# Kernel tuning notes

Hardware: AMD Instinct MI355X
Metric: run time of the kernel (lower is better)

## Reference

```python
import jax, jax.numpy as jnp
import numpy as np

EPS_BN = 1e-5
EPS_W = 1e-8


def setup_inputs() -> dict:
    key = jax.random.key(0)
    ks = jax.random.split(key, 6)
    B, N, S, D1, D2 = 8, 8192, 2048, 128, 256
    Cin = D1 + D2  # 384
    return {
        "points_position": jax.random.normal(ks[0], (B, 3, N), jnp.float32),
        "sampled_points_position": jax.random.normal(ks[1], (B, 3, S), jnp.float32),
        "skip_points_feature": jax.random.normal(ks[2], (B, D1, N), jnp.float32),
        "sampled_points_feature": jax.random.normal(ks[3], (B, D2, S), jnp.float32),
        "W1": jax.random.normal(ks[4], (256, Cin), jnp.float32) * 0.05,
        "b1": jnp.zeros((256,), jnp.float32),
        "g1": jnp.ones((256,), jnp.float32),
        "beta1": jnp.zeros((256,), jnp.float32),
        "W2": jax.random.normal(ks[5], (128, 256), jnp.float32) * 0.05,
        "b2": jnp.zeros((128,), jnp.float32),
        "g2": jnp.ones((128,), jnp.float32),
        "beta2": jnp.zeros((128,), jnp.float32),
    }


def _bn_relu(x, g, b):
    # train-mode BatchNorm1d over (batch, points) per channel, x: [B,N,C]
    mean = jnp.mean(x, axis=(0, 1), keepdims=True)
    var = jnp.mean(jnp.square(x - mean), axis=(0, 1), keepdims=True)  # biased var
    return jax.nn.relu((x - mean) * jax.lax.rsqrt(var + EPS_BN) * g + b)


def reference(points_position, sampled_points_position, skip_points_feature,
              sampled_points_feature, W1, b1, g1, beta1, W2, b2, g2, beta2):
    pos = points_position.transpose(0, 2, 1)            # [B,N,3]
    spos = sampled_points_position.transpose(0, 2, 1)   # [B,S,3]
    sfeat = sampled_points_feature.transpose(0, 2, 1)   # [B,S,D2]

    # squared pairwise distance [B,N,S]
    d = (jnp.sum(pos * pos, axis=-1, keepdims=True)
         - 2.0 * jnp.einsum("bnc,bsc->bns", pos, spos)
         + jnp.sum(spos * spos, axis=-1)[:, None, :])

    # 3 nearest neighbors (smallest distances)
    neg_d3, idx = jax.lax.top_k(-d, 3)                  # [B,N,3]
    d3 = -neg_d3
    w = 1.0 / (d3 + EPS_W)
    w = w / jnp.sum(w, axis=-1, keepdims=True)          # [B,N,3]

    gathered = jax.vmap(lambda f, i: f[i])(sfeat, idx)  # [B,N,3,D2]
    interp = jnp.einsum("bnk,bnkd->bnd", w, gathered)   # [B,N,D2]

    feat = jnp.concatenate([skip_points_feature.transpose(0, 2, 1), interp], axis=-1)  # [B,N,D1+D2]

    h = _bn_relu(jnp.einsum("bnc,oc->bno", feat, W1) + b1, g1, beta1)  # [B,N,256]
    h = _bn_relu(jnp.einsum("bnc,oc->bno", h, W2) + b2, g2, beta2)     # [B,N,128]
    return h.transpose(0, 2, 1)                          # [B,128,N]
```

## Files before the change

### kernel.cpp

```cpp
#include <hip/hip_runtime.h>

constexpr int BATCH = 8;
constexpr int NPT   = 8192;
constexpr int NSMP  = 2048;
constexpr int D1C   = 128;
constexpr int D2C   = 256;
constexpr int CIN   = 384;
constexpr int C1    = 256;
constexpr int C2    = 128;
constexpr int BN_TOTAL = BATCH * NPT;

constexpr int BM = 128, BK = 32;
constexpr int NRB = BN_TOTAL / BM;
constexpr int NRW = NRB * 2;

typedef __bf16 bf16x8 __attribute__((ext_vector_type(8)));
typedef short  s16x8  __attribute__((ext_vector_type(8)));
typedef float  f32x4  __attribute__((ext_vector_type(4)));

__device__ __forceinline__ unsigned short f2bf(float x) {
  unsigned u = __builtin_bit_cast(unsigned, x);
  u += 0x7fffu + ((u >> 16) & 1u);
  return (unsigned short)(u >> 16);
}
__device__ __forceinline__ float bf2f(unsigned short h) {
  return __builtin_bit_cast(float, (unsigned)h << 16);
}

__device__ __forceinline__ void gld_lds16(const void* g, void* l) {
  __builtin_amdgcn_global_load_lds(
      (const __attribute__((address_space(1))) void*)g,
      (__attribute__((address_space(3))) void*)l, 16, 0, 0);
}

__global__ void transpose_k(const float* __restrict__ in, float* __restrict__ out,
                            int rows, int cols, long inBatch, long outBatch) {
  __shared__ float tile[32][33];
  const float* inb = in + (size_t)blockIdx.z * inBatch;
  float* outb = out + (size_t)blockIdx.z * outBatch;
  int c0 = blockIdx.x * 32;
  int r0 = blockIdx.y * 32;
  int tx = threadIdx.x, ty = threadIdx.y;
#pragma unroll
  for (int i = 0; i < 32; i += 8) {
    int r = r0 + ty + i;
    tile[ty + i][tx] = inb[(size_t)r * cols + c0 + tx];
  }
  __syncthreads();
#pragma unroll
  for (int i = 0; i < 32; i += 8) {
    int c = c0 + ty + i;
    outb[(size_t)c * rows + r0 + tx] = tile[tx][ty + i];
  }
}

__global__ void skip_to_featB(const float* __restrict__ skip,
                              unsigned short* __restrict__ featB) {
  __shared__ float tile[32][33];
  int b = blockIdx.z;
  int n0 = blockIdx.x * 32;
  int d0 = blockIdx.y * 32;
  int tx = threadIdx.x, ty = threadIdx.y;
#pragma unroll
  for (int i = 0; i < 32; i += 8) {
    tile[ty + i][tx] = skip[((size_t)b * D1C + d0 + ty + i) * NPT + n0 + tx];
  }
  __syncthreads();
#pragma unroll
  for (int i = 0; i < 32; i += 8) {
    int n = n0 + ty + i;
    featB[((size_t)b * NPT + n) * CIN + d0 + tx] = f2bf(tile[tx][ty + i]);
  }
}

__global__ __launch_bounds__(256) void prep_misc(
    const float* __restrict__ spos, float* __restrict__ sposI, float4* __restrict__ qs4,
    const float* __restrict__ W1, unsigned short* __restrict__ W1h,
    const float* __restrict__ W2, unsigned short* __restrict__ W2h,
    int* __restrict__ flag_count) {
  int g = blockIdx.x * 256 + threadIdx.x;
  if (g == 0) *flag_count = 0;
  if (g < C1 * CIN) W1h[g] = f2bf(W1[g]);
  if (g < C2 * C1)  W2h[g] = f2bf(W2[g]);
  if (g < BATCH * NSMP) {
    int b = g >> 11, s = g & (NSMP - 1);
    const float* sp = spos + (size_t)b * 3 * NSMP;
    float x = sp[s], y = sp[NSMP + s], z = sp[2 * NSMP + s];
    sposI[(size_t)g * 3 + 0] = x;
    sposI[(size_t)g * 3 + 1] = y;
    sposI[(size_t)g * 3 + 2] = z;
    qs4[g] = make_float4(-2.f * x, -2.f * y, -2.f * z,
                         fmaf(x, x, fmaf(y, y, z * z)));
  }
}

constexpr int KWAVES = 8;
constexpr int SEGK = NSMP / KWAVES;

__device__ __forceinline__ void ins_med3(float kf, float& k0, float& k1,
                                         float& k2, float& k3) {
  float o0 = k0, o1 = k1, o2 = k2;
  k0 = fminf(kf, o0);
  k1 = __builtin_amdgcn_fmed3f(kf, o0, o1);
  k2 = __builtin_amdgcn_fmed3f(kf, o1, o2);
  k3 = __builtin_amdgcn_fmed3f(kf, o2, k3);
}

__global__ __launch_bounds__(512, 4) void knn_kernel(
    const float* __restrict__ pos,
    const float4* __restrict__ qs4g,
    const float* __restrict__ sposI,
    int* __restrict__ idx_out,
    float* __restrict__ wgt_out,
    int* __restrict__ flag_list,
    int* __restrict__ flag_count) {
  __shared__ float mk[KWAVES][4][64];

  int tid = threadIdx.x;
  int wave = tid >> 6, lane = tid & 63;
  int blk = blockIdx.x;
  int b = blk >> 7;
  int n = ((blk & 127) << 6) + lane;

  const float* pb = pos + (size_t)b * 3 * NPT;
  float px = pb[n], py = pb[NPT + n], pz = pb[2 * NPT + n];
  float pp = fmaf(px, px, fmaf(py, py, pz * pz));

  const float INF = __builtin_inff();
  float k0 = INF, k1 = INF, k2 = INF, k3 = INF;

  int s0 = wave * SEGK;
  int tv = 0;
  asm volatile("" : "+v"(tv));
  const float4* qseg = qs4g + (size_t)b * NSMP + s0 + tv;

#define KSTEP(Q, SS)                                                        \
  {                                                                         \
    float tt = (Q).w + pp;      \
    float d_ = fmaf(px, (Q).x, fmaf(py, (Q).y, fmaf(pz, (Q).z, tt)));       \
    unsigned ki_ = (__builtin_bit_cast(unsigned, d_) & 0xFFFFF800u) |       \
                   (unsigned)(SS);                                          \
    ins_med3(__builtin_bit_cast(float, ki_), k0, k1, k2, k3);               \
  }

  float4 qa[8], qb[8];
#pragma unroll
  for (int u = 0; u < 8; u++) qa[u] = qseg[u];
#pragma unroll
  for (int u = 0; u < 8; u++) qb[u] = qseg[8 + u];

  for (int t = 0; t < SEGK - 16; t += 16) {
    __builtin_amdgcn_sched_barrier(0);
#pragma unroll
    for (int u = 0; u < 8; u++) KSTEP(qa[u], s0 + t + u)
    __builtin_amdgcn_sched_barrier(0);
#pragma unroll
    for (int u = 0; u < 8; u++) qa[u] = qseg[t + 16 + u];
    __builtin_amdgcn_sched_barrier(0);
#pragma unroll
    for (int u = 0; u < 8; u++) KSTEP(qb[u], s0 + t + 8 + u)
    __builtin_amdgcn_sched_barrier(0);
#pragma unroll
    for (int u = 0; u < 8; u++) qb[u] = qseg[t + 24 + u];
  }
  __builtin_amdgcn_sched_barrier(0);
#pragma unroll
  for (int u = 0; u < 8; u++) KSTEP(qa[u], s0 + SEGK - 16 + u)
#pragma unroll
  for (int u = 0; u < 8; u++) KSTEP(qb[u], s0 + SEGK - 8 + u)
#undef KSTEP

  mk[wave][0][lane] = k0; mk[wave][1][lane] = k1;
  mk[wave][2][lane] = k2; mk[wave][3][lane] = k3;
  __syncthreads();

  if (tid < 64) {
    float K0 = INF, K1 = INF, K2 = INF, K3 = INF;
#pragma unroll
    for (int w = 0; w < KWAVES; w++)
#pragma unroll
      for (int sl = 0; sl < 4; sl++)
        ins_med3(mk[w][sl][tid], K0, K1, K2, K3);

    int p = blk * 64 + tid;
    int I0 = (int)(__builtin_bit_cast(unsigned, K0) & 0x7FFu);
    int I1 = (int)(__builtin_bit_cast(unsigned, K1) & 0x7FFu);
    int I2 = (int)(__builtin_bit_cast(unsigned, K2) & 0x7FFu);
    float d2m = __builtin_bit_cast(float, __builtin_bit_cast(unsigned, K2) & 0xFFFFF800u);
    float d3m = __builtin_bit_cast(float, __builtin_bit_cast(unsigned, K3) & 0xFFFFF800u);
    bool flag = (d3m - d2m) < 2e-3f * fmaxf(d3m, 0.f) + 1e-5f;
    if (flag) {
      int slot = atomicAdd(flag_count, 1);
      flag_list[slot] = p;
    }
    const float* q = sposI + (size_t)b * 3 * NSMP;
    double pxd = (double)px, pyd = (double)py, pzd = (double)pz;
    double dd[3]; int II[3] = {I0, I1, I2};
#pragma unroll
    for (int k = 0; k < 3; k++) {
      double dx = pxd - (double)q[3 * II[k]];
      double dy = pyd - (double)q[3 * II[k] + 1];
      double dz = pzd - (double)q[3 * II[k] + 2];
      dd[k] = dx * dx + dy * dy + dz * dz;
    }
    double w0 = 1.0 / (dd[0] + 1e-8);
    double w1 = 1.0 / (dd[1] + 1e-8);
    double w2 = 1.0 / (dd[2] + 1e-8);
    double inv = 1.0 / (w0 + w1 + w2);
    size_t o = (size_t)p * 3;
    idx_out[o + 0] = I0; idx_out[o + 1] = I1; idx_out[o + 2] = I2;
    wgt_out[o + 0] = (float)(w0 * inv);
    wgt_out[o + 1] = (float)(w1 * inv);
    wgt_out[o + 2] = (float)(w2 * inv);
  }
}

__device__ __forceinline__ bool dless(double d, int i, double D, int I) {
  return d < D || (d == D && i < I);
}
__device__ __forceinline__ void dins3(double d, int i,
                                      double& b0, double& b1, double& b2,
                                      int& i0, int& i1, int& i2) {
  if (dless(d, i, b2, i2)) {
    if (dless(d, i, b1, i1)) {
      b2 = b1; i2 = i1;
      if (dless(d, i, b0, i0)) { b1 = b0; i1 = i0; b0 = d; i0 = i; }
      else                     { b1 = d; i1 = i; }
    } else { b2 = d; i2 = i; }
  }
}

__global__ __launch_bounds__(256) void knn_fallback(
    const float* __restrict__ pos, const float* __restrict__ sposI,
    const int* __restrict__ flag_list, const int* __restrict__ flag_count,
    int* __restrict__ idx_out, float* __restrict__ wgt_out) {
  int wave = threadIdx.x >> 6, lane = threadIdx.x & 63;
  int gw = blockIdx.x * 4 + wave;
  int cnt = *flag_count;
  for (int t = gw; t < cnt; t += 1024) {
    int p = flag_list[t];
    int b = p >> 13, n = p & (NPT - 1);
    const float* pb = pos + (size_t)b * 3 * NPT;
    double px = (double)pb[n], py = (double)pb[NPT + n], pz = (double)pb[2 * NPT + n];
    const float* q = sposI + (size_t)b * 3 * NSMP;
    double b0 = 1e300, b1 = 1e300, b2 = 1e300;
    int i0 = 0x7FFFFFFF, i1 = 0x7FFFFFFF, i2 = 0x7FFFFFFF;
    for (int s = lane; s < NSMP; s += 64) {
      double dx = px - (double)q[3 * s];
      double dy = py - (double)q[3 * s + 1];
      double dz = pz - (double)q[3 * s + 2];
      double d = dx * dx + dy * dy + dz * dz;
      dins3(d, s, b0, b1, b2, i0, i1, i2);
    }
#pragma unroll
    for (int m = 1; m < 64; m <<= 1) {
      double o0 = __shfl_xor(b0, m, 64), o1 = __shfl_xor(b1, m, 64), o2 = __shfl_xor(b2, m, 64);
      int    j0 = __shfl_xor(i0, m, 64), j1 = __shfl_xor(i1, m, 64), j2 = __shfl_xor(i2, m, 64);
      dins3(o0, j0, b0, b1, b2, i0, i1, i2);
      dins3(o1, j1, b0, b1, b2, i0, i1, i2);
      dins3(o2, j2, b0, b1, b2, i0, i1, i2);
    }
    if (lane == 0) {
      double w0 = 1.0 / (b0 + 1e-8);
      double w1 = 1.0 / (b1 + 1e-8);
      double w2 = 1.0 / (b2 + 1e-8);
      double inv = 1.0 / (w0 + w1 + w2);
      size_t o = (size_t)p * 3;
      idx_out[o + 0] = i0; idx_out[o + 1] = i1; idx_out[o + 2] = i2;
      wgt_out[o + 0] = (float)(w0 * inv);
      wgt_out[o + 1] = (float)(w1 * inv);
      wgt_out[o + 2] = (float)(w2 * inv);
    }
  }
}

constexpr int IPB = 16;
__global__ __launch_bounds__(256) void interp_kernel(
    const float* __restrict__ sfeatT,
    const int* __restrict__ idx,
    const float* __restrict__ wgt,
    unsigned short* __restrict__ featB) {
  int c = threadIdx.x;
  int p0 = blockIdx.x * IPB;
  int b = p0 >> 13;
  const float* base = sfeatT + (size_t)b * NSMP * D2C;
#pragma unroll 4
  for (int pi = 0; pi < IPB; pi++) {
    int p = p0 + pi;
    size_t o = (size_t)p * 3;
    int i0 = idx[o], i1 = idx[o + 1], i2 = idx[o + 2];
    float w0 = wgt[o], w1 = wgt[o + 1], w2 = wgt[o + 2];
    float v = w0 * base[(size_t)i0 * D2C + c]
            + w1 * base[(size_t)i1 * D2C + c]
            + w2 * base[(size_t)i2 * D2C + c];
    featB[(size_t)p * CIN + D1C + c] = f2bf(v);
  }
}

__global__ __launch_bounds__(256) void gemm1_mw(
    const unsigned short* __restrict__ featB,
    const unsigned short* __restrict__ W1h,
    const float* __restrict__ bias,
    unsigned short* __restrict__ Y1,
    float* __restrict__ part_s,
    float* __restrict__ part_q) {
  __shared__ __align__(16) unsigned short As[BM * BK];
  __shared__ __align__(16) unsigned short Bs[BM * BK];
  int tid = threadIdx.x;
  int lane = tid & 63, w = tid >> 6;
  int wr = w >> 1, wc = w & 1;
  int m16 = lane & 15, quad = lane >> 4;
  int cb = blockIdx.x, rb = blockIdx.y;
  int row0 = rb * BM, col0 = cb * BM;
  int srow = lane >> 2, scol8 = (lane & 3) * 8;

  f32x4 acc[4][4];
#pragma unroll
  for (int j = 0; j < 4; j++) {
    float bj = bias[col0 + wc * 64 + j * 16 + m16];
#pragma unroll
    for (int i = 0; i < 4; i++) acc[i][j] = f32x4{bj, bj, bj, bj};
  }

  for (int k0 = 0; k0 < CIN; k0 += BK) {
#pragma unroll
    for (int kq = 0; kq < 2; kq++) {
      int ar = 32 * w + 16 * kq + srow;
      int lb = __builtin_amdgcn_readfirstlane((32 * w + 16 * kq) * BK);
      gld_lds16(&featB[(size_t)(row0 + ar) * CIN + k0 + scol8], &As[lb]);
      gld_lds16(&W1h[(size_t)(col0 + ar) * CIN + k0 + scol8], &Bs[lb]);
    }
    __syncthreads();

    bf16x8 a[4], bb[4];
#pragma unroll
    for (int i = 0; i < 4; i++)
      a[i] = __builtin_bit_cast(bf16x8,
          *(const s16x8*)&As[(wr * 64 + i * 16 + m16) * BK + quad * 8]);
#pragma unroll
    for (int j = 0; j < 4; j++)
      bb[j] = __builtin_bit_cast(bf16x8,
          *(const s16x8*)&Bs[(wc * 64 + j * 16 + m16) * BK + quad * 8]);
#pragma unroll
    for (int i = 0; i < 4; i++)
#pragma unroll
      for (int j = 0; j < 4; j++)
        acc[i][j] = __builtin_amdgcn_mfma_f32_16x16x32_bf16(a[i], bb[j], acc[i][j], 0, 0, 0);
    __syncthreads();
  }

#pragma unroll
  for (int j = 0; j < 4; j++) {
    int col = col0 + wc * 64 + j * 16 + m16;
    float s = 0.f, q = 0.f;
#pragma unroll
    for (int i = 0; i < 4; i++)
#pragma unroll
      for (int r = 0; r < 4; r++) {
        float v = acc[i][j][r];
        Y1[(size_t)(row0 + wr * 64 + i * 16 + quad * 4 + r) * C1 + col] = f2bf(v);
        s += v; q = fmaf(v, v, q);
      }
    s += __shfl_xor(s, 16, 64); s += __shfl_xor(s, 32, 64);
    q += __shfl_xor(q, 16, 64); q += __shfl_xor(q, 32, 64);
    if (quad == 0) {
      part_s[(size_t)col * NRW + rb * 2 + wr] = s;
      part_q[(size_t)col * NRW + rb * 2 + wr] = q;
    }
  }
}

__global__ __launch_bounds__(256) void gemm2_mw(
    const unsigned short* __restrict__ Y1,
    const float* __restrict__ scale1, const float* __restrict__ shift1,
    const unsigned short* __restrict__ W2h,
    const float* __restrict__ bias,
    unsigned short* __restrict__ Y2,
    float* __restrict__ part_s,
    float* __restrict__ part_q) {
  __shared__ __align__(16) unsigned short As[BM * BK];
  __shared__ __align__(16) unsigned short Bs[BM * BK];
  __shared__ float scs[C1], shs[C1];
  int tid = threadIdx.x;
  int lane = tid & 63, w = tid >> 6;
  int wr = w >> 1, wc = w & 1;
  int m16 = lane & 15, quad = lane >> 4;
  int rb = blockIdx.x;
  int row0 = rb * BM, col0 = 0;
  int srow = lane >> 2, scol8 = (lane & 3) * 8;

  scs[tid] = scale1[tid]; shs[tid] = shift1[tid];

  f32x4 acc[4][4];
#pragma unroll
  for (int j = 0; j < 4; j++) {
    float bj = bias[col0 + wc * 64 + j * 16 + m16];
#pragma unroll
    for (int i = 0; i < 4; i++) acc[i][j] = f32x4{bj, bj, bj, bj};
  }
  __syncthreads();

  for (int k0 = 0; k0 < C1; k0 += BK) {
#pragma unroll
    for (int kq = 0; kq < 2; kq++) {
      int ar = 32 * w + 16 * kq + srow;
      int lb = __builtin_amdgcn_readfirstlane((32 * w + 16 * kq) * BK);
      gld_lds16(&W2h[(size_t)(col0 + ar) * C1 + k0 + scol8], &Bs[lb]);
      s16x8 v = *(const s16x8*)&Y1[(size_t)(row0 + ar) * C1 + k0 + scol8];
      unsigned short ov[8];
#pragma unroll
      for (int e = 0; e < 8; e++) {
        float x = bf2f((unsigned short)v[e]);
        float y = fmaxf(fmaf(x, scs[k0 + scol8 + e], shs[k0 + scol8 + e]), 0.f);
        ov[e] = f2bf(y);
      }
      *(s16x8*)&As[ar * BK + scol8] = *(const s16x8*)ov;
    }
    __syncthreads();

    bf16x8 a[4], bb[4];
#pragma unroll
    for (int i = 0; i < 4; i++)
      a[i] = __builtin_bit_cast(bf16x8,
          *(const s16x8*)&As[(wr * 64 + i * 16 + m16) * BK + quad * 8]);
#pragma unroll
    for (int j = 0; j < 4; j++)
      bb[j] = __builtin_bit_cast(bf16x8,
          *(const s16x8*)&Bs[(wc * 64 + j * 16 + m16) * BK + quad * 8]);
#pragma unroll
    for (int i = 0; i < 4; i++)
#pragma unroll
      for (int j = 0; j < 4; j++)
        acc[i][j] = __builtin_amdgcn_mfma_f32_16x16x32_bf16(a[i], bb[j], acc[i][j], 0, 0, 0);
    __syncthreads();
  }

#pragma unroll
  for (int j = 0; j < 4; j++) {
    int col = col0 + wc * 64 + j * 16 + m16;
    float s = 0.f, q = 0.f;
#pragma unroll
    for (int i = 0; i < 4; i++)
#pragma unroll
      for (int r = 0; r < 4; r++) {
        float v = acc[i][j][r];
        Y2[(size_t)(row0 + wr * 64 + i * 16 + quad * 4 + r) * C2 + col] = f2bf(v);
        s += v; q = fmaf(v, v, q);
      }
    s += __shfl_xor(s, 16, 64); s += __shfl_xor(s, 32, 64);
    q += __shfl_xor(q, 16, 64); q += __shfl_xor(q, 32, 64);
    if (quad == 0) {
      part_s[(size_t)col * NRW + rb * 2 + wr] = s;
      part_q[(size_t)col * NRW + rb * 2 + wr] = q;
    }
  }
}

__global__ __launch_bounds__(256) void bn_reduce_coef(
    const float* __restrict__ part_s, const float* __restrict__ part_q, int nrb,
    const float* __restrict__ g, const float* __restrict__ beta,
    float* __restrict__ scale, float* __restrict__ shift) {
  int ch = blockIdx.x;
  int tid = threadIdx.x;
  float s = 0.f, q = 0.f;
  for (int t = tid; t < nrb; t += 256) {
    s += part_s[(size_t)ch * nrb + t];
    q += part_q[(size_t)ch * nrb + t];
  }
#pragma unroll
  for (int m = 1; m < 64; m <<= 1) {
    s += __shfl_xor(s, m, 64);
    q += __shfl_xor(q, m, 64);
  }
  __shared__ float ls[4], lq[4];
  int wave = tid >> 6;
  if ((tid & 63) == 0) { ls[wave] = s; lq[wave] = q; }
  __syncthreads();
  if (tid == 0) {
    s = ls[0] + ls[1] + ls[2] + ls[3];
    q = lq[0] + lq[1] + lq[2] + lq[3];
    const float invBN = 1.0f / (float)BN_TOTAL;
    float mean = s * invBN;
    float var = q * invBN - mean * mean;
    float sc = g[ch] / sqrtf(var + 1e-5f);
    scale[ch] = sc;
    shift[ch] = beta[ch] - mean * sc;
  }
}

__global__ void final_kernel(const unsigned short* __restrict__ Y2,
                             const float* __restrict__ scale, const float* __restrict__ shift,
                             float* __restrict__ out) {
  __shared__ float tile[32][33];
  int b = blockIdx.z;
  int n0 = blockIdx.x * 32;
  int c0 = blockIdx.y * 32;
  int tx = threadIdx.x, ty = threadIdx.y;
  float sc = scale[c0 + tx];
  float sh = shift[c0 + tx];
#pragma unroll
  for (int i = 0; i < 32; i += 8) {
    int n = n0 + ty + i;
    float v = bf2f(Y2[((size_t)b * NPT + n) * C2 + c0 + tx]);
    tile[ty + i][tx] = fmaxf(fmaf(v, sc, sh), 0.f);
  }
  __syncthreads();
#pragma unroll
  for (int i = 0; i < 32; i += 8) {
    int c = c0 + ty + i;
    out[((size_t)b * C2 + c) * NPT + n0 + tx] = tile[tx][ty + i];
  }
}

extern "C" void kernel_launch(void* const* d_in, const int* in_sizes, int n_in,
                              void* d_out, int out_size, void* d_ws, size_t ws_size,
                              hipStream_t stream) {
  (void)in_sizes; (void)n_in; (void)out_size; (void)ws_size;
  const float* pos   = (const float*)d_in[0];
  const float* spos  = (const float*)d_in[1];
  const float* skip  = (const float*)d_in[2];
  const float* sfeat = (const float*)d_in[3];
  const float* W1    = (const float*)d_in[4];
  const float* b1    = (const float*)d_in[5];
  const float* g1    = (const float*)d_in[6];
  const float* beta1 = (const float*)d_in[7];
  const float* W2    = (const float*)d_in[8];
  const float* b2    = (const float*)d_in[9];
  const float* g2    = (const float*)d_in[10];
  const float* beta2 = (const float*)d_in[11];
  float* out = (float*)d_out;

  float* ws = (float*)d_ws;
  size_t off = 0;
  float* sfeatT  = ws + off; off += (size_t)BATCH * NSMP * D2C;
  unsigned short* featB = (unsigned short*)(ws + off); off += (size_t)BN_TOTAL * CIN / 2;
  unsigned short* Y1    = (unsigned short*)(ws + off); off += (size_t)BN_TOTAL * C1 / 2;
  unsigned short* Y2    = (unsigned short*)(ws + off); off += (size_t)BN_TOTAL * C2 / 2;
  unsigned short* W1h   = (unsigned short*)(ws + off); off += (size_t)C1 * CIN / 2;
  unsigned short* W2h   = (unsigned short*)(ws + off); off += (size_t)C2 * C1 / 2;
  int*   knn_idx = (int*)(ws + off); off += (size_t)BN_TOTAL * 3;
  float* knn_w   = ws + off; off += (size_t)BN_TOTAL * 3;
  float* sposI   = ws + off; off += (size_t)BATCH * NSMP * 3;
  float4* qs4    = (float4*)(ws + off); off += (size_t)BATCH * NSMP * 4;
  int* flag_list = (int*)(ws + off); off += (size_t)BN_TOTAL;
  float* part1_s = ws + off; off += (size_t)C1 * NRW;
  float* part1_q = ws + off; off += (size_t)C1 * NRW;
  float* part2_s = ws + off; off += (size_t)C2 * NRW;
  float* part2_q = ws + off; off += (size_t)C2 * NRW;
  float* stats   = ws + off; off += 2048;
  int*   flag_count = (int*)stats;
  float* scale1 = stats + 256, *shift1 = stats + 512;
  float* scale2 = stats + 768, *shift2 = stats + 1024;

  dim3 tb(32, 8);
  prep_misc<<<(C1 * CIN + 255) / 256, 256, 0, stream>>>(
      spos, sposI, qs4, W1, W1h, W2, W2h, flag_count);
  transpose_k<<<dim3(NSMP / 32, D2C / 32, BATCH), tb, 0, stream>>>(
      sfeat, sfeatT, D2C, NSMP, (long)D2C * NSMP, (long)NSMP * D2C);
  skip_to_featB<<<dim3(NPT / 32, D1C / 32, BATCH), tb, 0, stream>>>(skip, featB);

  knn_kernel<<<BN_TOTAL / 64, 512, 0, stream>>>(pos, qs4, sposI, knn_idx, knn_w,
                                                flag_list, flag_count);
  knn_fallback<<<256, 256, 0, stream>>>(pos, sposI, flag_list, flag_count,
                                        knn_idx, knn_w);
  interp_kernel<<<BN_TOTAL / IPB, 256, 0, stream>>>(sfeatT, knn_idx, knn_w, featB);

  gemm1_mw<<<dim3(C1 / BM, NRB), 256, 0, stream>>>(
      featB, W1h, b1, Y1, part1_s, part1_q);
  bn_reduce_coef<<<C1, 256, 0, stream>>>(part1_s, part1_q, NRW, g1, beta1, scale1, shift1);

  gemm2_mw<<<NRB, 256, 0, stream>>>(
      Y1, scale1, shift1, W2h, b2, Y2, part2_s, part2_q);
  bn_reduce_coef<<<C2, 256, 0, stream>>>(part2_s, part2_q, NRW, g2, beta2, scale2, shift2);

  final_kernel<<<dim3(NPT / 32, C2 / 32, BATCH), tb, 0, stream>>>(Y2, scale2, shift2, out);
}
```

Measured before the change: 297.2 us.

## Fuse prep, kNN, fallback, interpolation and BN-reduction kernels to cut launches

Merges the three preprocessing kernels into one launch, and folds the kNN search, the exact fallback (now handled per block through a shared-memory flag list) and the feature interpolation into a single knn_all kernel. Each thread now handles four query points so every sample load is reused across them. The BN statistic reductions move into the tails of the GEMM kernels using a last-block atomic counter, and the interpolation switches to float4 vectorized gathers. This removes several launches and the global idx/weight round trip, at the cost of higher register pressure in the kNN loop and a serial final reduction done by a single block.

```diff
diff --git a/kernel.cpp b/kernel.cpp
--- a/kernel.cpp
+++ b/kernel.cpp
@@ -17,6 +17,7 @@
 typedef __bf16 bf16x8 __attribute__((ext_vector_type(8)));
 typedef short  s16x8  __attribute__((ext_vector_type(8)));
 typedef float  f32x4  __attribute__((ext_vector_type(4)));
+typedef unsigned short u16x4 __attribute__((ext_vector_type(4)));
 
 __device__ __forceinline__ unsigned short f2bf(float x) {
   unsigned u = __builtin_bit_cast(unsigned, x);
@@ -33,64 +34,65 @@
       (__attribute__((address_space(3))) void*)l, 16, 0, 0);
 }
 
-__global__ void transpose_k(const float* __restrict__ in, float* __restrict__ out,
-                            int rows, int cols, long inBatch, long outBatch) {
-  __shared__ float tile[32][33];
-  const float* inb = in + (size_t)blockIdx.z * inBatch;
-  float* outb = out + (size_t)blockIdx.z * outBatch;
-  int c0 = blockIdx.x * 32;
-  int r0 = blockIdx.y * 32;
-  int tx = threadIdx.x, ty = threadIdx.y;
-#pragma unroll
-  for (int i = 0; i < 32; i += 8) {
-    int r = r0 + ty + i;
-    tile[ty + i][tx] = inb[(size_t)r * cols + c0 + tx];
-  }
-  __syncthreads();
-#pragma unroll
-  for (int i = 0; i < 32; i += 8) {
-    int c = c0 + ty + i;
-    outb[(size_t)c * rows + r0 + tx] = tile[tx][ty + i];
-  }
-}
-
-__global__ void skip_to_featB(const float* __restrict__ skip,
-                              unsigned short* __restrict__ featB) {
-  __shared__ float tile[32][33];
-  int b = blockIdx.z;
-  int n0 = blockIdx.x * 32;
-  int d0 = blockIdx.y * 32;
-  int tx = threadIdx.x, ty = threadIdx.y;
-#pragma unroll
-  for (int i = 0; i < 32; i += 8) {
-    tile[ty + i][tx] = skip[((size_t)b * D1C + d0 + ty + i) * NPT + n0 + tx];
-  }
-  __syncthreads();
-#pragma unroll
-  for (int i = 0; i < 32; i += 8) {
-    int n = n0 + ty + i;
-    featB[((size_t)b * NPT + n) * CIN + d0 + tx] = f2bf(tile[tx][ty + i]);
-  }
-}
-
-__global__ __launch_bounds__(256) void prep_misc(
-    const float* __restrict__ spos, float* __restrict__ sposI, float4* __restrict__ qs4,
+constexpr int PT_T = (NSMP / 32) * (D2C / 32) * BATCH;
+constexpr int PT_S = (NPT / 32) * (D1C / 32) * BATCH;
+constexpr int PT_M = (C1 * CIN + 255) / 256;
+
+__global__ __launch_bounds__(256) void prep_all(
+    const float* __restrict__ sfeat, float* __restrict__ sfeatT,
+    const float* __restrict__ skip, unsigned short* __restrict__ featB,
+    const float* __restrict__ spos, float* __restrict__ sposI,
+    float4* __restrict__ qs4,
     const float* __restrict__ W1, unsigned short* __restrict__ W1h,
     const float* __restrict__ W2, unsigned short* __restrict__ W2h,
-    int* __restrict__ flag_count) {
-  int g = blockIdx.x * 256 + threadIdx.x;
-  if (g == 0) *flag_count = 0;
-  if (g < C1 * CIN) W1h[g] = f2bf(W1[g]);
-  if (g < C2 * C1)  W2h[g] = f2bf(W2[g]);
-  if (g < BATCH * NSMP) {
-    int b = g >> 11, s = g & (NSMP - 1);
-    const float* sp = spos + (size_t)b * 3 * NSMP;
-    float x = sp[s], y = sp[NSMP + s], z = sp[2 * NSMP + s];
-    sposI[(size_t)g * 3 + 0] = x;
-    sposI[(size_t)g * 3 + 1] = y;
-    sposI[(size_t)g * 3 + 2] = z;
-    qs4[g] = make_float4(-2.f * x, -2.f * y, -2.f * z,
-                         fmaf(x, x, fmaf(y, y, z * z)));
+    int* __restrict__ ctrs) {
+  __shared__ float tile[32][33];
+  int bid = blockIdx.x, tid = threadIdx.x;
+  int tx = tid & 31, ty = tid >> 5;
+  if (bid < PT_T) {
+    int z = bid >> 9;
+    int r = bid & 511;
+    int c0 = (r & 63) * 32;
+    int r0 = (r >> 6) * 32;
+    const float* inb = sfeat + (size_t)z * D2C * NSMP;
+    float* outb = sfeatT + (size_t)z * NSMP * D2C;
+#pragma unroll
+    for (int i = 0; i < 32; i += 8)
+      tile[ty + i][tx] = inb[(size_t)(r0 + ty + i) * NSMP + c0 + tx];
+    __syncthreads();
+#pragma unroll
+    for (int i = 0; i < 32; i += 8)
+      outb[(size_t)(c0 + ty + i) * D2C + r0 + tx] = tile[tx][ty + i];
+  } else if (bid < PT_T + PT_S) {
+    int id = bid - PT_T;
+    int z = id >> 10;
+    int r = id & 1023;
+    int n0 = (r & 255) * 32;
+    int d0 = (r >> 8) * 32;
+#pragma unroll
+    for (int i = 0; i < 32; i += 8)
+      tile[ty + i][tx] = skip[((size_t)z * D1C + d0 + ty + i) * NPT + n0 + tx];
+    __syncthreads();
+#pragma unroll
+    for (int i = 0; i < 32; i += 8) {
+      int n = n0 + ty + i;
+      featB[((size_t)z * NPT + n) * CIN + d0 + tx] = f2bf(tile[tx][ty + i]);
+    }
+  } else {
+    int g = (bid - PT_T - PT_S) * 256 + tid;
+    if (g == 0) { ctrs[0] = 0; ctrs[1] = 0; }
+    if (g < C1 * CIN) W1h[g] = f2bf(W1[g]);
+    if (g < C2 * C1)  W2h[g] = f2bf(W2[g]);
+    if (g < BATCH * NSMP) {
+      int b = g >> 11, s = g & (NSMP - 1);
+      const float* sp = spos + (size_t)b * 3 * NSMP;
+      float x = sp[s], y = sp[NSMP + s], z = sp[2 * NSMP + s];
+      sposI[(size_t)g * 3 + 0] = x;
+      sposI[(size_t)g * 3 + 1] = y;
+      sposI[(size_t)g * 3 + 2] = z;
+      qs4[g] = make_float4(-2.f * x, -2.f * y, -2.f * z,
+                           fmaf(x, x, fmaf(y, y, z * z)));
+    }
   }
 }
 
@@ -104,115 +106,6 @@
   k1 = __builtin_amdgcn_fmed3f(kf, o0, o1);
   k2 = __builtin_amdgcn_fmed3f(kf, o1, o2);
   k3 = __builtin_amdgcn_fmed3f(kf, o2, k3);
-}
-
-__global__ __launch_bounds__(512, 4) void knn_kernel(
-    const float* __restrict__ pos,
-    const float4* __restrict__ qs4g,
-    const float* __restrict__ sposI,
-    int* __restrict__ idx_out,
-    float* __restrict__ wgt_out,
-    int* __restrict__ flag_list,
-    int* __restrict__ flag_count) {
-  __shared__ float mk[KWAVES][4][64];
-
-  int tid = threadIdx.x;
-  int wave = tid >> 6, lane = tid & 63;
-  int blk = blockIdx.x;
-  int b = blk >> 7;
-  int n = ((blk & 127) << 6) + lane;
-
-  const float* pb = pos + (size_t)b * 3 * NPT;
-  float px = pb[n], py = pb[NPT + n], pz = pb[2 * NPT + n];
-  float pp = fmaf(px, px, fmaf(py, py, pz * pz));
-
-  const float INF = __builtin_inff();
-  float k0 = INF, k1 = INF, k2 = INF, k3 = INF;
-
-  int s0 = wave * SEGK;
-  int tv = 0;
-  asm volatile("" : "+v"(tv));
-  const float4* qseg = qs4g + (size_t)b * NSMP + s0 + tv;
-
-#define KSTEP(Q, SS)                                                        \
-  {                                                                         \
-    float tt = (Q).w + pp;      \
-    float d_ = fmaf(px, (Q).x, fmaf(py, (Q).y, fmaf(pz, (Q).z, tt)));       \
-    unsigned ki_ = (__builtin_bit_cast(unsigned, d_) & 0xFFFFF800u) |       \
-                   (unsigned)(SS);                                          \
-    ins_med3(__builtin_bit_cast(float, ki_), k0, k1, k2, k3);               \
-  }
-
-  float4 qa[8], qb[8];
-#pragma unroll
-  for (int u = 0; u < 8; u++) qa[u] = qseg[u];
-#pragma unroll
-  for (int u = 0; u < 8; u++) qb[u] = qseg[8 + u];
-
-  for (int t = 0; t < SEGK - 16; t += 16) {
-    __builtin_amdgcn_sched_barrier(0);
-#pragma unroll
-    for (int u = 0; u < 8; u++) KSTEP(qa[u], s0 + t + u)
-    __builtin_amdgcn_sched_barrier(0);
-#pragma unroll
-    for (int u = 0; u < 8; u++) qa[u] = qseg[t + 16 + u];
-    __builtin_amdgcn_sched_barrier(0);
-#pragma unroll
-    for (int u = 0; u < 8; u++) KSTEP(qb[u], s0 + t + 8 + u)
-    __builtin_amdgcn_sched_barrier(0);
-#pragma unroll
-    for (int u = 0; u < 8; u++) qb[u] = qseg[t + 24 + u];
-  }
-  __builtin_amdgcn_sched_barrier(0);
-#pragma unroll
-  for (int u = 0; u < 8; u++) KSTEP(qa[u], s0 + SEGK - 16 + u)
-#pragma unroll
-  for (int u = 0; u < 8; u++) KSTEP(qb[u], s0 + SEGK - 8 + u)
-#undef KSTEP
-
-  mk[wave][0][lane] = k0; mk[wave][1][lane] = k1;
-  mk[wave][2][lane] = k2; mk[wave][3][lane] = k3;
-  __syncthreads();
-
-  if (tid < 64) {
-    float K0 = INF, K1 = INF, K2 = INF, K3 = INF;
-#pragma unroll
-    for (int w = 0; w < KWAVES; w++)
-#pragma unroll
-      for (int sl = 0; sl < 4; sl++)
-        ins_med3(mk[w][sl][tid], K0, K1, K2, K3);
-
-    int p = blk * 64 + tid;
-    int I0 = (int)(__builtin_bit_cast(unsigned, K0) & 0x7FFu);
-    int I1 = (int)(__builtin_bit_cast(unsigned, K1) & 0x7FFu);
-    int I2 = (int)(__builtin_bit_cast(unsigned, K2) & 0x7FFu);
-    float d2m = __builtin_bit_cast(float, __builtin_bit_cast(unsigned, K2) & 0xFFFFF800u);
-    float d3m = __builtin_bit_cast(float, __builtin_bit_cast(unsigned, K3) & 0xFFFFF800u);
-    bool flag = (d3m - d2m) < 2e-3f * fmaxf(d3m, 0.f) + 1e-5f;
-    if (flag) {
-      int slot = atomicAdd(flag_count, 1);
-      flag_list[slot] = p;
-    }
-    const float* q = sposI + (size_t)b * 3 * NSMP;
-    double pxd = (double)px, pyd = (double)py, pzd = (double)pz;
-    double dd[3]; int II[3] = {I0, I1, I2};
-#pragma unroll
-    for (int k = 0; k < 3; k++) {
-      double dx = pxd - (double)q[3 * II[k]];
-      double dy = pyd - (double)q[3 * II[k] + 1];
-      double dz = pzd - (double)q[3 * II[k] + 2];
-      dd[k] = dx * dx + dy * dy + dz * dz;
-    }
-    double w0 = 1.0 / (dd[0] + 1e-8);
-    double w1 = 1.0 / (dd[1] + 1e-8);
-    double w2 = 1.0 / (dd[2] + 1e-8);
-    double inv = 1.0 / (w0 + w1 + w2);
-    size_t o = (size_t)p * 3;
-    idx_out[o + 0] = I0; idx_out[o + 1] = I1; idx_out[o + 2] = I2;
-    wgt_out[o + 0] = (float)(w0 * inv);
-    wgt_out[o + 1] = (float)(w1 * inv);
-    wgt_out[o + 2] = (float)(w2 * inv);
-  }
 }
 
 __device__ __forceinline__ bool dless(double d, int i, double D, int I) {
@@ -230,25 +123,147 @@
   }
 }
 
-__global__ __launch_bounds__(256) void knn_fallback(
-    const float* __restrict__ pos, const float* __restrict__ sposI,
-    const int* __restrict__ flag_list, const int* __restrict__ flag_count,
-    int* __restrict__ idx_out, float* __restrict__ wgt_out) {
-  int wave = threadIdx.x >> 6, lane = threadIdx.x & 63;
-  int gw = blockIdx.x * 4 + wave;
-  int cnt = *flag_count;
-  for (int t = gw; t < cnt; t += 1024) {
-    int p = flag_list[t];
-    int b = p >> 13, n = p & (NPT - 1);
-    const float* pb = pos + (size_t)b * 3 * NPT;
-    double px = (double)pb[n], py = (double)pb[NPT + n], pz = (double)pb[2 * NPT + n];
+__global__ __launch_bounds__(512, 4) void knn_all(
+    const float* __restrict__ pos,
+    const float4* __restrict__ qs4g,
+    const float* __restrict__ sposI,
+    const float* __restrict__ sfeatT,
+    unsigned short* __restrict__ featB) {
+  __shared__ float mk[KWAVES][4][4][64];
+  __shared__ int   il[256][3];
+  __shared__ float wl[256][3];
+  __shared__ int   fl[256];
+  __shared__ int   fcnt;
+
+  int tid = threadIdx.x;
+  int wave = tid >> 6, lane = tid & 63;
+  int blk = blockIdx.x;
+  int b = blk >> 5;
+  int n0 = (blk & 31) << 8;
+
+  if (tid == 0) fcnt = 0;
+
+  const float* pb = pos + (size_t)b * 3 * NPT;
+  float px[4], py[4], pz[4], pp[4];
+#pragma unroll
+  for (int m = 0; m < 4; m++) {
+    int n = n0 + (m << 6) + lane;
+    px[m] = pb[n]; py[m] = pb[NPT + n]; pz[m] = pb[2 * NPT + n];
+    pp[m] = fmaf(px[m], px[m], fmaf(py[m], py[m], pz[m] * pz[m]));
+  }
+
+  const float INF = __builtin_inff();
+  float k0[4], k1[4], k2[4], k3[4];
+#pragma unroll
+  for (int m = 0; m < 4; m++) { k0[m] = INF; k1[m] = INF; k2[m] = INF; k3[m] = INF; }
+
+  int s0 = wave * SEGK;
+  int tv = 0;
+  asm volatile("" : "+v"(tv));
+  const float4* qseg = qs4g + (size_t)b * NSMP + s0 + tv;
+
+#define KSTEP4(Q, SS)                                                        \
+  {                                                                          \
+    _Pragma("unroll")                                                        \
+    for (int m_ = 0; m_ < 4; m_++) {                                         \
+      float tt = (Q).w + pp[m_];       \
+      float d_ = fmaf(px[m_], (Q).x,                                         \
+                      fmaf(py[m_], (Q).y, fmaf(pz[m_], (Q).z, tt)));         \
+      unsigned ki_ = (__builtin_bit_cast(unsigned, d_) & 0xFFFFF800u) |      \
+                     (unsigned)(SS);                                         \
+      ins_med3(__builtin_bit_cast(float, ki_), k0[m_], k1[m_], k2[m_], k3[m_]); \
+    }                                                                        \
+  }
+
+  float4 qa[4], qb[4];
+#pragma unroll
+  for (int u = 0; u < 4; u++) qa[u] = qseg[u];
+#pragma unroll
+  for (int u = 0; u < 4; u++) qb[u] = qseg[4 + u];
+
+  for (int t = 0; t < SEGK - 8; t += 8) {
+    __builtin_amdgcn_sched_barrier(0);
+#pragma unroll
+    for (int u = 0; u < 4; u++) KSTEP4(qa[u], s0 + t + u)
+    __builtin_amdgcn_sched_barrier(0);
+#pragma unroll
+    for (int u = 0; u < 4; u++) qa[u] = qseg[t + 8 + u];
+    __builtin_amdgcn_sched_barrier(0);
+#pragma unroll
+    for (int u = 0; u < 4; u++) KSTEP4(qb[u], s0 + t + 4 + u)
+    __builtin_amdgcn_sched_barrier(0);
+#pragma unroll
+    for (int u = 0; u < 4; u++) qb[u] = qseg[t + 12 + u];
+  }
+  __builtin_amdgcn_sched_barrier(0);
+#pragma unroll
+  for (int u = 0; u < 4; u++) KSTEP4(qa[u], s0 + SEGK - 8 + u)
+#pragma unroll
+  for (int u = 0; u < 4; u++) KSTEP4(qb[u], s0 + SEGK - 4 + u)
+#undef KSTEP4
+
+#pragma unroll
+  for (int m = 0; m < 4; m++) {
+    mk[wave][0][m][lane] = k0[m];
+    mk[wave][1][m][lane] = k1[m];
+    mk[wave][2][m][lane] = k2[m];
+    mk[wave][3][m][lane] = k3[m];
+  }
+  __syncthreads();
+
+  if (tid < 256) {
+    int pm = tid >> 6, pl = tid & 63;
+    float K0 = INF, K1 = INF, K2 = INF, K3 = INF;
+#pragma unroll
+    for (int w = 0; w < KWAVES; w++)
+#pragma unroll
+      for (int sl = 0; sl < 4; sl++)
+        ins_med3(mk[w][sl][pm][pl], K0, K1, K2, K3);
+
+    int I0 = (int)(__builtin_bit_cast(unsigned, K0) & 0x7FFu);
+    int I1 = (int)(__builtin_bit_cast(unsigned, K1) & 0x7FFu);
+    int I2 = (int)(__builtin_bit_cast(unsigned, K2) & 0x7FFu);
+    float d2m = __builtin_bit_cast(float, __builtin_bit_cast(unsigned, K2) & 0xFFFFF800u);
+    float d3m = __builtin_bit_cast(float, __builtin_bit_cast(unsigned, K3) & 0xFFFFF800u);
+    bool flag = (d3m - d2m) < 2e-3f * fmaxf(d3m, 0.f) + 1e-5f;
+    if (flag) {
+      int slot = atomicAdd(&fcnt, 1);
+      fl[slot] = tid;
+    }
+    int n = n0 + tid;
+    const float* q = sposI + (size_t)b * 3 * NSMP;
+    double pxd = (double)pb[n], pyd = (double)pb[NPT + n], pzd = (double)pb[2 * NPT + n];
+    double dd[3]; int II[3] = {I0, I1, I2};
+#pragma unroll
+    for (int k = 0; k < 3; k++) {
+      double dx = pxd - (double)q[3 * II[k]];
+      double dy = pyd - (double)q[3 * II[k] + 1];
+      double dz = pzd - (double)q[3 * II[k] + 2];
+      dd[k] = dx * dx + dy * dy + dz * dz;
+    }
+    double w0 = 1.0 / (dd[0] + 1e-8);
+    double w1 = 1.0 / (dd[1] + 1e-8);
+    double w2 = 1.0 / (dd[2] + 1e-8);
+    double inv = 1.0 / (w0 + w1 + w2);
+    il[tid][0] = I0; il[tid][1] = I1; il[tid][2] = I2;
+    wl[tid][0] = (float)(w0 * inv);
+    wl[tid][1] = (float)(w1 * inv);
+    wl[tid][2] = (float)(w2 * inv);
+  }
+  __syncthreads();
+
+  int fc = fcnt;
+  for (int t = wave; t < fc; t += KWAVES) {
+    int P = fl[t];
+    int n = n0 + P;
+    double pxd = (double)pb[n], pyd = (double)pb[NPT + n], pzd = (double)pb[2 * NPT + n];
     const float* q = sposI + (size_t)b * 3 * NSMP;
     double b0 = 1e300, b1 = 1e300, b2 = 1e300;
     int i0 = 0x7FFFFFFF, i1 = 0x7FFFFFFF, i2 = 0x7FFFFFFF;
     for (int s = lane; s < NSMP; s += 64) {
-      double dx = px - (double)q[3 * s];
-      double dy = py - (double)q[3 * s + 1];
-      double dz = pz - (double)q[3 * s + 2];
+      double dx = pxd - (double)q[3 * s];
+      double dy = pyd - (double)q[3 * s + 1];
+      double dz = pzd - (double)q[3 * s + 2];
       double d = dx * dx + dy * dy + dz * dz;
       dins3(d, s, b0, b1, b2, i0, i1, i2);
     }
@@ -265,35 +280,28 @@
       double w1 = 1.0 / (b1 + 1e-8);
       double w2 = 1.0 / (b2 + 1e-8);
       double inv = 1.0 / (w0 + w1 + w2);
-      size_t o = (size_t)p * 3;
-      idx_out[o + 0] = i0; idx_out[o + 1] = i1; idx_out[o + 2] = i2;
-      wgt_out[o + 0] = (float)(w0 * inv);
-      wgt_out[o + 1] = (float)(w1 * inv);
-      wgt_out[o + 2] = (float)(w2 * inv);
-    }
-  }
-}
-
-constexpr int IPB = 16;
-__global__ __launch_bounds__(256) void interp_kernel(
-    const float* __restrict__ sfeatT,
-    const int* __restrict__ idx,
-    const float* __restrict__ wgt,
-    unsigned short* __restrict__ featB) {
-  int c = threadIdx.x;
-  int p0 = blockIdx.x * IPB;
-  int b = p0 >> 13;
+      il[P][0] = i0; il[P][1] = i1; il[P][2] = i2;
+      wl[P][0] = (float)(w0 * inv);
+      wl[P][1] = (float)(w1 * inv);
+      wl[P][2] = (float)(w2 * inv);
+    }
+  }
+  __syncthreads();
+
   const float* base = sfeatT + (size_t)b * NSMP * D2C;
-#pragma unroll 4
-  for (int pi = 0; pi < IPB; pi++) {
-    int p = p0 + pi;
-    size_t o = (size_t)p * 3;
-    int i0 = idx[o], i1 = idx[o + 1], i2 = idx[o + 2];
-    float w0 = wgt[o], w1 = wgt[o + 1], w2 = wgt[o + 2];
-    float v = w0 * base[(size_t)i0 * D2C + c]
-            + w1 * base[(size_t)i1 * D2C + c]
-            + w2 * base[(size_t)i2 * D2C + c];
-    featB[(size_t)p * CIN + D1C + c] = f2bf(v);
+  for (int i = 0; i < 32; i++) {
+    int P = (wave << 5) + i;
+    int i0 = il[P][0], i1 = il[P][1], i2 = il[P][2];
+    float w0 = wl[P][0], w1 = wl[P][1], w2 = wl[P][2];
+    float4 v0 = *(const float4*)&base[(size_t)i0 * D2C + (lane << 2)];
+    float4 v1 = *(const float4*)&base[(size_t)i1 * D2C + (lane << 2)];
+    float4 v2 = *(const float4*)&base[(size_t)i2 * D2C + (lane << 2)];
+    u16x4 o;
+    o[0] = f2bf(w0 * v0.x + w1 * v1.x + w2 * v2.x);
+    o[1] = f2bf(w0 * v0.y + w1 * v1.y + w2 * v2.y);
+    o[2] = f2bf(w0 * v0.z + w1 * v1.z + w2 * v2.z);
+    o[3] = f2bf(w0 * v0.w + w1 * v1.w + w2 * v2.w);
+    *(u16x4*)&featB[((size_t)b * NPT + n0 + P) * CIN + D1C + (lane << 2)] = o;
   }
 }
 
@@ -303,7 +311,10 @@
     const float* __restrict__ bias,
     unsigned short* __restrict__ Y1,
     float* __restrict__ part_s,
-    float* __restrict__ part_q) {
+    float* __restrict__ part_q,
+    const float* __restrict__ g1, const float* __restrict__ beta1,
+    float* __restrict__ scale1, float* __restrict__ shift1,
+    int* __restrict__ ctr) {
   __shared__ __align__(16) unsigned short As[BM * BK];
   __shared__ __align__(16) unsigned short Bs[BM * BK];
   int tid = threadIdx.x;
@@ -368,6 +379,30 @@
       part_q[(size_t)col * NRW + rb * 2 + wr] = q;
     }
   }
+
+  __threadfence();
+  __shared__ int isLast;
+  if (tid == 0)
+    isLast = (atomicAdd(ctr, 1) == (int)(gridDim.x * gridDim.y) - 1);
+  __syncthreads();
+  if (isLast) {
+    __threadfence();
+    int ch = tid;
+    const float4* ps = (const float4*)&part_s[(size_t)ch * NRW];
+    const float4* pq = (const float4*)&part_q[(size_t)ch * NRW];
+    float s = 0.f, q = 0.f;
+    for (int t = 0; t < NRW / 4; t++) {
+      float4 a = ps[t], c = pq[t];
+      s += a.x + a.y + a.z + a.w;
+      q += c.x + c.y + c.z + c.w;
+    }
+    const float invBN = 1.0f / (float)BN_TOTAL;
+    float mean = s * invBN;
+    float var = q * invBN - mean * mean;
+    float sc = g1[ch] / sqrtf(var + 1e-5f);
+    scale1[ch] = sc;
+    shift1[ch] = beta1[ch] - mean * sc;
+  }
 }
 
 __global__ __launch_bounds__(256) void gemm2_mw(
@@ -377,7 +412,10 @@
     const float* __restrict__ bias,
     unsigned short* __restrict__ Y2,
     float* __restrict__ part_s,
-    float* __restrict__ part_q) {
+    float* __restrict__ part_q,
+    const float* __restrict__ g2, const float* __restrict__ beta2,
+    float* __restrict__ scale2, float* __restrict__ shift2,
+    int* __restrict__ ctr) {
   __shared__ __align__(16) unsigned short As[BM * BK];
   __shared__ __align__(16) unsigned short Bs[BM * BK];
   __shared__ float scs[C1], shs[C1];
@@ -454,37 +492,28 @@
       part_q[(size_t)col * NRW + rb * 2 + wr] = q;
     }
   }
-}
-
-__global__ __launch_bounds__(256) void bn_reduce_coef(
-    const float* __restrict__ part_s, const float* __restrict__ part_q, int nrb,
-    const float* __restrict__ g, const float* __restrict__ beta,
-    float* __restrict__ scale, float* __restrict__ shift) {
-  int ch = blockIdx.x;
-  int tid = threadIdx.x;
-  float s = 0.f, q = 0.f;
-  for (int t = tid; t < nrb; t += 256) {
-    s += part_s[(size_t)ch * nrb + t];
-    q += part_q[(size_t)ch * nrb + t];
-  }
-#pragma unroll
-  for (int m = 1; m < 64; m <<= 1) {
-    s += __shfl_xor(s, m, 64);
-    q += __shfl_xor(q, m, 64);
-  }
-  __shared__ float ls[4], lq[4];
-  int wave = tid >> 6;
-  if ((tid & 63) == 0) { ls[wave] = s; lq[wave] = q; }
-  __syncthreads();
-  if (tid == 0) {
-    s = ls[0] + ls[1] + ls[2] + ls[3];
-    q = lq[0] + lq[1] + lq[2] + lq[3];
+
+  __threadfence();
+  __shared__ int isLast;
+  if (tid == 0) isLast = (atomicAdd(ctr, 1) == (int)gridDim.x - 1);
+  __syncthreads();
+  if (isLast && tid < C2) {
+    __threadfence();
+    int ch = tid;
+    const float4* ps = (const float4*)&part_s[(size_t)ch * NRW];
+    const float4* pq = (const float4*)&part_q[(size_t)ch * NRW];
+    float s = 0.f, q = 0.f;
+    for (int t = 0; t < NRW / 4; t++) {
+      float4 a = ps[t], c = pq[t];
+      s += a.x + a.y + a.z + a.w;
+      q += c.x + c.y + c.z + c.w;
+    }
     const float invBN = 1.0f / (float)BN_TOTAL;
     float mean = s * invBN;
     float var = q * invBN - mean * mean;
-    float sc = g[ch] / sqrtf(var + 1e-5f);
-    scale[ch] = sc;
-    shift[ch] = beta[ch] - mean * sc;
+    float sc = g2[ch] / sqrtf(var + 1e-5f);
+    scale2[ch] = sc;
+    shift2[ch] = beta2[ch] - mean * sc;
   }
 }
 
@@ -538,40 +567,29 @@
   unsigned short* Y2    = (unsigned short*)(ws + off); off += (size_t)BN_TOTAL * C2 / 2;
   unsigned short* W1h   = (unsigned short*)(ws + off); off += (size_t)C1 * CIN / 2;
   unsigned short* W2h   = (unsigned short*)(ws + off); off += (size_t)C2 * C1 / 2;
-  int*   knn_idx = (int*)(ws + off); off += (size_t)BN_TOTAL * 3;
-  float* knn_w   = ws + off; off += (size_t)BN_TOTAL * 3;
   float* sposI   = ws + off; off += (size_t)BATCH * NSMP * 3;
   float4* qs4    = (float4*)(ws + off); off += (size_t)BATCH * NSMP * 4;
-  int* flag_list = (int*)(ws + off); off += (size_t)BN_TOTAL;
   float* part1_s = ws + off; off += (size_t)C1 * NRW;
   float* part1_q = ws + off; off += (size_t)C1 * NRW;
   float* part2_s = ws + off; off += (size_t)C2 * NRW;
   float* part2_q = ws + off; off += (size_t)C2 * NRW;
   float* stats   = ws + off; off += 2048;
-  int*   flag_count = (int*)stats;
+  int*   ctrs    = (int*)stats;
   float* scale1 = stats + 256, *shift1 = stats + 512;
   float* scale2 = stats + 768, *shift2 = stats + 1024;
 
-  dim3 tb(32, 8);
-  prep_misc<<<(C1 * CIN + 255) / 256, 256, 0, stream>>>(
-      spos, sposI, qs4, W1, W1h, W2, W2h, flag_count);
-  transpose_k<<<dim3(NSMP / 32, D2C / 32, BATCH), tb, 0, stream>>>(
-      sfeat, sfeatT, D2C, NSMP, (long)D2C * NSMP, (long)NSMP * D2C);
-  skip_to_featB<<<dim3(NPT / 32, D1C / 32, BATCH), tb, 0, stream>>>(skip, featB);
-
-  knn_kernel<<<BN_TOTAL / 64, 512, 0, stream>>>(pos, qs4, sposI, knn_idx, knn_w,
-                                                flag_list, flag_count);
-  knn_fallback<<<256, 256, 0, stream>>>(pos, sposI, flag_list, flag_count,
-                                        knn_idx, knn_w);
-  interp_kernel<<<BN_TOTAL / IPB, 256, 0, stream>>>(sfeatT, knn_idx, knn_w, featB);
+  prep_all<<<PT_T + PT_S + PT_M, 256, 0, stream>>>(
+      sfeat, sfeatT, skip, featB, spos, sposI, qs4, W1, W1h, W2, W2h, ctrs);
+
+  knn_all<<<BN_TOTAL / 256, 512, 0, stream>>>(pos, qs4, sposI, sfeatT, featB);
 
   gemm1_mw<<<dim3(C1 / BM, NRB), 256, 0, stream>>>(
-      featB, W1h, b1, Y1, part1_s, part1_q);
-  bn_reduce_coef<<<C1, 256, 0, stream>>>(part1_s, part1_q, NRW, g1, beta1, scale1, shift1);
+      featB, W1h, b1, Y1, part1_s, part1_q, g1, beta1, scale1, shift1, &ctrs[0]);
 
   gemm2_mw<<<NRB, 256, 0, stream>>>(
-      Y1, scale1, shift1, W2h, b2, Y2, part2_s, part2_q);
-  bn_reduce_coef<<<C2, 256, 0, stream>>>(part2_s, part2_q, NRW, g2, beta2, scale2, shift2);
-
-  final_kernel<<<dim3(NPT / 32, C2 / 32, BATCH), tb, 0, stream>>>(Y2, scale2, shift2, out);
-}
+      Y1, scale1, shift1, W2h, b2, Y2, part2_s, part2_q,
+      g2, beta2, scale2, shift2, &ctrs[1]);
+
+  final_kernel<<<dim3(NPT / 32, C2 / 32, BATCH), dim3(32, 8), 0, stream>>>(
+      Y2, scale2, shift2, out);
+}
```

Result: slower. 601.6 us (+102.4%).
